# Optimization experiments

Measured on AMD Instinct MI355X. Metric: run time of the kernel, lower is better.

Reference implementation:

```python
import jax, jax.numpy as jnp
import numpy as np

WS = 7  # window size


def _rel_pos_index(ws):
    coords = np.stack(np.meshgrid(np.arange(ws), np.arange(ws), indexing='ij')).reshape(2, -1)
    rel = (coords[:, :, None] - coords[:, None, :]).transpose(1, 2, 0)  # (N,N,2)
    rel[..., 0] += ws - 1
    rel[..., 1] += ws - 1
    rel[..., 0] *= 2 * ws - 1
    return jnp.asarray(rel.sum(-1))  # (N,N) int


def setup_inputs() -> dict:
    key = jax.random.key(0)
    ks = jax.random.split(key, 10)
    B, DIM, H, W, NH = 16, 256, 56, 56, 8
    HD = DIM // NH
    x = jax.random.normal(ks[0], (B, DIM, H, W), jnp.float32)
    qkv_w = jax.random.normal(ks[1], (DIM, 3 * DIM), jnp.float32) * 0.02
    qkv_b = jnp.zeros((3 * DIM,), jnp.float32)
    fc_w = jax.random.normal(ks[2], (9, 3 * NH), jnp.float32) * 0.1
    fc_b = jnp.zeros((9,), jnp.float32)
    base = np.zeros((9, 3, 3), np.float32)
    for i in range(9):
        base[i, i // 3, i % 3] = 1.0
    dep_w = jnp.asarray(np.broadcast_to(base, (DIM, 9, 3, 3)).copy()) \
        + jax.random.normal(ks[3], (DIM, 9, 3, 3), jnp.float32) * 0.01
    proj_w = jax.random.normal(ks[4], (DIM, DIM), jnp.float32) * 0.02
    proj_b = jnp.zeros((DIM,), jnp.float32)
    rpb_table = jax.random.normal(ks[5], ((2 * WS - 1) * (2 * WS - 1), NH), jnp.float32) * 0.02
    rate1 = jnp.full((1,), 0.5, jnp.float32)
    rate2 = jnp.full((1,), 0.5, jnp.float32)
    return dict(x=x, qkv_w=qkv_w, qkv_b=qkv_b, fc_w=fc_w, fc_b=fc_b, dep_w=dep_w,
                proj_w=proj_w, proj_b=proj_b, rpb_table=rpb_table, rate1=rate1, rate2=rate2)


def reference(x, qkv_w, qkv_b, fc_w, fc_b, dep_w, proj_w, proj_b, rpb_table, rate1, rate2):
    B, DIM, H, W = x.shape
    NH = fc_w.shape[1] // 3
    HD = DIM // NH
    N = WS * WS
    xp = jnp.transpose(x, (0, 2, 3, 1))              # (B,H,W,C)
    qkv = xp @ qkv_w + qkv_b                          # (B,H,W,3C)

    # ----- conv branch -----
    f_all = qkv.reshape(B, H * W, 3 * NH, HD)         # (B,HW,3NH,HD)
    fc_out = jnp.einsum('oc,bncd->bnod', fc_w, f_all) + fc_b[None, None, :, None]  # (B,HW,9,HD)
    # torch channel layout: (B, HD, 9, HW) -> (B, 9*HD, H, W) with hd-major ordering
    f_conv = jnp.transpose(fc_out, (0, 3, 2, 1)).reshape(B, 9 * HD, H, W)
    out_conv = jax.lax.conv_general_dilated(
        f_conv, dep_w, window_strides=(1, 1), padding=((1, 1), (1, 1)),
        feature_group_count=HD, dimension_numbers=('NCHW', 'OIHW', 'NCHW'))  # (B,C,H,W)
    out_conv = jnp.transpose(out_conv, (0, 2, 3, 1))  # (B,H,W,C)

    # ----- window attention branch -----
    w = qkv.reshape(B, H // WS, WS, W // WS, WS, 3 * DIM)
    w = jnp.transpose(w, (0, 1, 3, 2, 4, 5)).reshape(-1, N, 3 * DIM)  # (B_,N,3C)
    B_ = w.shape[0]
    w = w.reshape(B_, N, 3, NH, HD)
    q, k, v = jnp.transpose(w, (2, 0, 3, 1, 4))       # each (B_,NH,N,HD)
    scale = HD ** -0.5
    attn = jnp.einsum('bhnd,bhmd->bhnm', q * scale, k)  # (B_,NH,N,N)
    idx = _rel_pos_index(WS)
    bias = jnp.transpose(rpb_table[idx.reshape(-1)].reshape(N, N, NH), (2, 0, 1))  # (NH,N,N)
    attn = jax.nn.softmax(attn + bias[None], axis=-1)
    o = jnp.einsum('bhnm,bhmd->bnhd', attn, v).reshape(B_, N, DIM)
    o = o @ proj_w.T + proj_b                          # torch Linear: y = x W^T + b
    o = o.reshape(B_, WS, WS, DIM)
    o = o.reshape(B, H // WS, W // WS, WS, WS, DIM)
    o = jnp.transpose(o, (0, 1, 3, 2, 4, 5)).reshape(B, H, W, DIM)

    out = rate1 * o + rate2 * out_conv
    return jnp.transpose(out, (0, 3, 1, 2))           # (B,C,H,W)
```

## Files before the change

### kernel.cpp

```cpp
#include <hip/hip_runtime.h>

#define BATCH 16
#define DIM 256
#define HH 56
#define WW 56
#define HWP 3136
#define M_TOT 50176
#define NQKV 768
#define NHEADS 8
#define HDIM 32
#define NWIN 49
#define QKV_BYTES   77070336ull
#define XT_OFF      77070336ull
#define XT_BYTES    25690112ull
#define WQT_OFF    102760448ull
#define PWB_OFF    103153664ull
#define FCONV_OFF  103284736ull
#define BIAS_OFF   132186112ull

typedef float f32x4 __attribute__((ext_vector_type(4)));
typedef short short8 __attribute__((ext_vector_type(8)));
typedef unsigned short ushort4v __attribute__((ext_vector_type(4)));

__device__ __forceinline__ short f2bf(float f) {
    unsigned u = __float_as_uint(f);
    u += 0x7fffu + ((u >> 16) & 1u);
    return (short)(u >> 16);
}
__device__ __forceinline__ float bf2f(unsigned short u) {
    return __uint_as_float(((unsigned)u) << 16);
}
__device__ __forceinline__ unsigned pack2bf(float lo, float hi) {
    unsigned ul = __float_as_uint(lo); ul += 0x7fffu + ((ul >> 16) & 1u);
    unsigned uh = __float_as_uint(hi); uh += 0x7fffu + ((uh >> 16) & 1u);
    return (ul >> 16) | (uh & 0xffff0000u);
}
__device__ __forceinline__ int div7(int n) { return (n * 9363) >> 16; }

__device__ __forceinline__ void gld16(const unsigned short* g, unsigned short* l) {
    __builtin_amdgcn_global_load_lds(
        (const __attribute__((address_space(1))) void*)g,
        (__attribute__((address_space(3))) void*)l, 16, 0, 0);
}

__global__ __launch_bounds__(256) void xpose_kernel(const float* __restrict__ x,
                                                    unsigned short* __restrict__ xt) {
    __shared__ unsigned short tls[64 * 448];
    const int tid = threadIdx.x;
    const int p0 = blockIdx.x * 448;
    const int k0 = blockIdx.y * 64;
    const int b  = blockIdx.z;
    const float* xb = x + ((size_t)b * DIM + k0) * HWP + p0;
    #pragma unroll
    for (int pass = 0; pass < 28; ++pass) {
        int idx = tid + pass * 256;
        int ch = idx / 112, px4 = idx - ch * 112;
        float4 v = *(const float4*)(xb + (size_t)ch * HWP + px4 * 4);
        int px4s = px4 ^ ((ch >> 3) & 7);
        ushort4v s;
        s[0] = (unsigned short)f2bf(v.x); s[1] = (unsigned short)f2bf(v.y);
        s[2] = (unsigned short)f2bf(v.z); s[3] = (unsigned short)f2bf(v.w);
        *(ushort4v*)&tls[ch * 448 + px4s * 4] = s;
    }
    __syncthreads();
    unsigned short* xto = xt + ((size_t)b * HWP + p0) * DIM + k0;
    #pragma unroll
    for (int q = 0; q < 14; ++q) {
        int idx = tid + q * 256;
        int px = idx >> 3, j8 = (idx & 7) * 8;
        int key = (j8 >> 3) & 7;
        int pxs = ((px >> 2) ^ key) * 4 + (px & 3);
        unsigned r[4];
        #pragma unroll
        for (int jj = 0; jj < 4; ++jj) {
            unsigned lo = tls[(j8 + 2 * jj) * 448 + pxs];
            unsigned hi = tls[(j8 + 2 * jj + 1) * 448 + pxs];
            r[jj] = lo | (hi << 16);
        }
        uint4 o; o.x = r[0]; o.y = r[1]; o.z = r[2]; o.w = r[3];
        *(uint4*)(xto + (size_t)px * DIM + j8) = o;
    }
}

__global__ __launch_bounds__(256) void prep_kernel(const float* __restrict__ wq,
                                                   const float* __restrict__ pw,
                                                   const float* __restrict__ rpb,
                                                   unsigned short* __restrict__ wqt,
                                                   unsigned short* __restrict__ pwb,
                                                   float* __restrict__ biasT) {
    const int tid = threadIdx.x;
    const int bid = blockIdx.x;
    if (bid < 48) {
        __shared__ float t[64][65];
        const int j0 = (bid >> 2) * 64, k0 = (bid & 3) * 64;
        #pragma unroll
        for (int kk = tid >> 6; kk < 64; kk += 4)
            t[kk][tid & 63] = wq[(size_t)(k0 + kk) * NQKV + j0 + (tid & 63)];
        __syncthreads();
        const int jj = tid >> 2, c16 = (tid & 3) * 16;
        unsigned short* dst = wqt + (size_t)(j0 + jj) * DIM + k0 + c16;
        #pragma unroll
        for (int i = 0; i < 16; ++i) dst[i] = (unsigned short)f2bf(t[c16 + i][jj]);
    } else if (bid < 64) {
        const int base = (bid - 48) * 4096 + tid;
        #pragma unroll
        for (int i = 0; i < 16; ++i)
            pwb[base + i * 256] = (unsigned short)f2bf(pw[base + i * 256]);
    } else {
        const int h = bid - 64;
        #pragma unroll
        for (int i = 0; i < 16; ++i) {
            int idx = tid + i * 256;
            int n = idx >> 6, m = idx & 63;
            float v = -1e30f;
            if (n < 49 && m < 49) {
                int nd = div7(n), md = div7(m);
                int ii = (nd - md + 6) * 13 + ((n - nd * 7) - (m - md * 7) + 6);
                v = rpb[ii * NHEADS + h] * 1.4426950408889634f;
            }
            biasT[h * 4096 + idx] = v;
        }
    }
}

__global__ __launch_bounds__(256) void qkv_gemm(const unsigned short* __restrict__ xt,
                                                const unsigned short* __restrict__ wqt,
                                                const float* __restrict__ bq,
                                                unsigned short* __restrict__ qkv) {
    __shared__ __attribute__((aligned(16))) short A_lds[2][128 * 32];
    __shared__ __attribute__((aligned(16))) short B_lds[2][128 * 32];
    const int bidx = blockIdx.x;
    const int wg = (bidx & 7) * 294 + (bidx >> 3);
    const int jt = wg % 6, mt = wg / 6;
    const int m0 = mt * 128, j0 = jt * 128;

    const int tid = threadIdx.x;
    const int lane = tid & 63;
    const int wave = tid >> 6;
    const int wr = wave >> 1, wc = wave & 1;
    const int r = lane & 15, q = lane >> 4;

    const unsigned short* aG[2];
    const unsigned short* bG[2];
    int lbase[2];
    #pragma unroll
    for (int t = 0; t < 2; ++t) {
        int ci = wave * 128 + t * 64 + lane;
        int srow = ci >> 2;
        int kgrp = (ci & 3) ^ (srow & 3);
        aG[t] = xt  + (size_t)(m0 + srow) * DIM + kgrp * 8;
        bG[t] = wqt + (size_t)(j0 + srow) * DIM + kgrp * 8;
        lbase[t] = (wave * 128 + t * 64) * 8;
    }

    f32x4 acc[4][4];
    #pragma unroll
    for (int i = 0; i < 4; ++i)
        #pragma unroll
        for (int j = 0; j < 4; ++j) acc[i][j] = (f32x4){0.f, 0.f, 0.f, 0.f};

    #pragma unroll
    for (int t = 0; t < 2; ++t) {
        gld16(aG[t], (unsigned short*)&A_lds[0][lbase[t]]);
        gld16(bG[t], (unsigned short*)&B_lds[0][lbase[t]]);
    }
    __syncthreads();

    #pragma unroll
    for (int k = 0; k < 8; ++k) {
        const int buf = k & 1;
        if (k < 7) {
            const int k0 = (k + 1) * 32;
            #pragma unroll
            for (int t = 0; t < 2; ++t) {
                gld16(aG[t] + k0, (unsigned short*)&A_lds[buf ^ 1][lbase[t]]);
                gld16(bG[t] + k0, (unsigned short*)&B_lds[buf ^ 1][lbase[t]]);
            }
        }
        short8 af[4], bfr[4];
        #pragma unroll
        for (int f = 0; f < 4; ++f) {
            int mrow = wr * 64 + f * 16 + r;
            af[f] = *(const short8*)&A_lds[buf][mrow * 32 + 8 * (q ^ (mrow & 3))];
            int nrow = wc * 64 + f * 16 + r;
            bfr[f] = *(const short8*)&B_lds[buf][nrow * 32 + 8 * (q ^ (nrow & 3))];
        }
        #pragma unroll
        for (int fm = 0; fm < 4; ++fm)
            #pragma unroll
            for (int fj = 0; fj < 4; ++fj)
                acc[fm][fj] = __builtin_amdgcn_mfma_f32_16x16x32_bf16(
                    af[fm], bfr[fj], acc[fm][fj], 0, 0, 0);
        __syncthreads();
    }

    #pragma unroll
    for (int fm = 0; fm < 4; ++fm) {
        const int mbase = m0 + wr * 64 + fm * 16 + q * 4;
        #pragma unroll
        for (int fj = 0; fj < 4; ++fj) {
            const int j = j0 + wc * 64 + fj * 16 + r;
            const float bias = bq[j];
            unsigned short* op = qkv + (size_t)mbase * NQKV + j;
            #pragma unroll
            for (int rg = 0; rg < 4; ++rg)
                op[(size_t)rg * NQKV] = (unsigned short)f2bf(acc[fm][fj][rg] + bias);
        }
    }
}

__global__ __launch_bounds__(256) void fc_kernel(const unsigned short* __restrict__ qkv,
                                                 const float* __restrict__ fc_w,
                                                 const float* __restrict__ fc_b,
                                                 unsigned short* __restrict__ fconv) {
    __shared__ unsigned short f[16 * 768];
    __shared__ float ob[16][289];
    __shared__ float w[9][24];
    __shared__ float bsh[9];
    const int tid = threadIdx.x;
    if (tid < 216) w[tid / 24][tid % 24] = fc_w[tid];
    if (tid < 9) bsh[tid] = fc_b[tid];
    const int p0 = blockIdx.x * 16;
    const int b  = blockIdx.y;
    const uint4* src = (const uint4*)(qkv + ((size_t)b * HWP + p0) * NQKV);
    uint4* dstf = (uint4*)f;
    #pragma unroll
    for (int i = 0; i < 6; ++i) dstf[tid + i * 256] = src[tid + i * 256];
    __syncthreads();
    #pragma unroll
    for (int it = 0; it < 2; ++it) {
        const int item = tid + it * 256;
        const int pp = item >> 5, g = item & 31;
        const unsigned short* fr = f + pp * 768 + g;
        float acc[9];
        #pragma unroll
        for (int o = 0; o < 9; ++o) acc[o] = bsh[o];
        #pragma unroll
        for (int c = 0; c < 24; ++c) {
            float v = bf2f(fr[c * 32]);
            #pragma unroll
            for (int o = 0; o < 9; ++o) acc[o] += w[o][c] * v;
        }
        #pragma unroll
        for (int o = 0; o < 9; ++o) ob[pp][g * 9 + o] = acc[o];
    }
    __syncthreads();
    unsigned short* og = fconv + (size_t)b * 288 * HWP + p0;
    for (int i = tid; i < 288 * 16; i += 256) {
        int ch = i >> 4, pp = i & 15;
        og[(size_t)ch * HWP + pp] = (unsigned short)f2bf(ob[pp][ch]);
    }
}

__global__ __launch_bounds__(256) void conv_kernel(const unsigned short* __restrict__ fconv,
                                                   const float* __restrict__ dep_w,
                                                   const float* __restrict__ rate2p,
                                                   float* __restrict__ out) {
    __shared__ unsigned short hal[9][10][64];
    __shared__ float wfl[81][8];
    const int tid = threadIdx.x;
    const int strip = blockIdx.x;
    const int g = blockIdx.y, b = blockIdx.z;

    for (int i = tid; i < 648; i += 256) {
        int ok = i >> 3, c8 = i & 7;
        wfl[ok][c8] = dep_w[(size_t)(g * 8 + c8) * 81 + ok];
    }
    const unsigned short* fp = fconv + ((size_t)b * 288 + g * 9) * HWP;
    const int y0 = strip * 8 - 1;
    for (int i = tid; i < 5760; i += 256) {
        int col = i & 63;
        int rest = i >> 6;
        int o = rest / 10, y = rest - o * 10;
        int gy = y0 + y, gx = col - 1;
        unsigned short v = 0;
        if (gy >= 0 && gy < HH && (unsigned)gx < WW)
            v = fp[(size_t)o * HWP + gy * WW + gx];
        hal[o][y][col] = v;
    }
    __syncthreads();

    const int x = tid & 63;
    const int w = tid >> 6;
    const int e = x & ~1;
    const bool odd = (x & 1) != 0;
    float acc[2][8] = {};
    for (int o = 0; o < 9; ++o) {
        float V[4][3];
        #pragma unroll
        for (int h = 0; h < 4; ++h) {
            const unsigned short* hr = &hal[o][2 * w + h][e];
            unsigned D0 = *(const unsigned*)hr;
            unsigned D1 = *(const unsigned*)(hr + 2);
            float a0 = __uint_as_float(D0 << 16);
            float a1 = __uint_as_float(D0 & 0xffff0000u);
            float a2 = __uint_as_float(D1 << 16);
            float a3 = __uint_as_float(D1 & 0xffff0000u);
            V[h][0] = odd ? a1 : a0;
            V[h][1] = odd ? a2 : a1;
            V[h][2] = odd ? a3 : a2;
        }
        #pragma unroll
        for (int ky = 0; ky < 3; ++ky)
            #pragma unroll
            for (int kx = 0; kx < 3; ++kx) {
                f32x4 w0 = *(const f32x4*)&wfl[o * 9 + ky * 3 + kx][0];
                f32x4 w1 = *(const f32x4*)&wfl[o * 9 + ky * 3 + kx][4];
                #pragma unroll
                for (int j = 0; j < 2; ++j) {
                    const float vv = V[j + ky][kx];
                    acc[j][0] += vv * w0[0]; acc[j][1] += vv * w0[1];
                    acc[j][2] += vv * w0[2]; acc[j][3] += vv * w0[3];
                    acc[j][4] += vv * w1[0]; acc[j][5] += vv * w1[1];
                    acc[j][6] += vv * w1[2]; acc[j][7] += vv * w1[3];
                }
            }
    }
    if (x < WW) {
        const float r2 = rate2p[0];
        #pragma unroll
        for (int j = 0; j < 2; ++j) {
            const int y = strip * 8 + 2 * w + j;
            #pragma unroll
            for (int c8 = 0; c8 < 8; ++c8)
                out[((size_t)b * DIM + g * 8 + c8) * HWP + y * WW + x] = r2 * acc[j][c8];
        }
    }
}

__global__ __launch_bounds__(512) void attn_kernel(const unsigned short* __restrict__ qkv,
                                                   const float* __restrict__ biasT,
                                                   unsigned short* __restrict__ obuf) {
    __shared__ __attribute__((aligned(16))) short PL[8 * 16 * 72];
    const int tid = threadIdx.x;
    const int win = blockIdx.x;
    const int b = win >> 6, wrw = win & 63;
    const int wy = wrw >> 3, wx = wrw & 7;
    const size_t wbase = (size_t)b * HWP + (size_t)(wy * 7) * WW + wx * 7;

    const int lane = tid & 63;
    const int h = tid >> 6;
    const int c = lane & 15, qg = lane >> 4;

    short8 aq[4], bk[4];
    #pragma unroll
    for (int f = 0; f < 4; ++f) {
        int t = f * 16 + c; if (t > 48) t = 48;
        const int tq = div7(t), tr = t - tq * 7;
        const unsigned short* base = qkv + (wbase + tq * WW + tr) * NQKV + h * 32 + qg * 8;
        aq[f] = *(const short8*)base;
        bk[f] = *(const short8*)(base + 256);
    }
    short8 bv[2][2];
    #pragma unroll
    for (int ks = 0; ks < 2; ++ks)
        #pragma unroll
        for (int i = 0; i < 8; ++i) {
            int pix = ks * 32 + qg * 8 + i; if (pix > 48) pix = 48;
            const int pd = div7(pix);
            const unsigned short* vp = qkv + (wbase + pd * WW + (pix - pd * 7)) * NQKV
                                           + 512 + h * 32 + c;
            bv[ks][0][i] = (short)vp[0];
            bv[ks][1][i] = (short)vp[16];
        }

    const float cst = 0.25503766727f;
    const float* bt = biasT + h * 4096;
    short* pw = PL + h * 16 * 72;

    #pragma unroll
    for (int fm = 0; fm < 4; ++fm) {
        f32x4 s[4];
        #pragma unroll
        for (int fj = 0; fj < 4; ++fj)
            s[fj] = __builtin_amdgcn_mfma_f32_16x16x32_bf16(aq[fm], bk[fj],
                                                            (f32x4){0.f,0.f,0.f,0.f}, 0, 0, 0);
        float p[4][4];
        #pragma unroll
        for (int reg = 0; reg < 4; ++reg) {
            const float* brow = bt + (fm * 16 + qg * 4 + reg) * 64;
            #pragma unroll
            for (int fj = 0; fj < 4; ++fj)
                p[fj][reg] = exp2f(s[fj][reg] * cst + brow[fj * 16 + c]);
        }
        float inv[4];
        #pragma unroll
        for (int reg = 0; reg < 4; ++reg) {
            float sum = (p[0][reg] + p[1][reg]) + (p[2][reg] + p[3][reg]);
            sum += __shfl_xor(sum, 1);
            sum += __shfl_xor(sum, 2);
            sum += __shfl_xor(sum, 4);
            sum += __shfl_xor(sum, 8);
            inv[reg] = 1.0f / sum;
        }
        #pragma unroll
        for (int fj = 0; fj < 4; ++fj)
            #pragma unroll
            for (int reg = 0; reg < 4; ++reg) {
                float v = p[fj][reg];
                float o = __shfl_xor(v, 1);
                unsigned packed = (c & 1) ? pack2bf(o, v) : pack2bf(v, o);
                if ((c & 1) == 0)
                    *(unsigned*)&pw[(qg * 4 + reg) * 72 + fj * 16 + c] = packed;
            }
        short8 ap0 = *(const short8*)&pw[c * 72 + 0 * 32 + qg * 8];
        short8 ap1 = *(const short8*)&pw[c * 72 + 1 * 32 + qg * 8];
        #pragma unroll
        for (int fo = 0; fo < 2; ++fo) {
            f32x4 o4 = __builtin_amdgcn_mfma_f32_16x16x32_bf16(ap0, bv[0][fo],
                                                               (f32x4){0.f,0.f,0.f,0.f}, 0, 0, 0);
            o4 = __builtin_amdgcn_mfma_f32_16x16x32_bf16(ap1, bv[1][fo], o4, 0, 0, 0);
            #pragma unroll
            for (int reg = 0; reg < 4; ++reg) {
                int n = fm * 16 + qg * 4 + reg;
                if (n < 49) {
                    int nd = div7(n), nm = n - nd * 7;
                    obuf[(wbase + nd * WW + nm) * DIM + h * 32 + fo * 16 + c] =
                        (unsigned short)f2bf(o4[reg] * inv[reg]);
                }
            }
        }
    }
}

__global__ __launch_bounds__(256) void proj_gemm(const unsigned short* __restrict__ obuf,
                                                 const unsigned short* __restrict__ pwb,
                                                 const float* __restrict__ pb,
                                                 const float* __restrict__ rate1p,
                                                 float* __restrict__ out) {
    __shared__ __attribute__((aligned(16))) short M_lds[2][128 * 32];
    __shared__ __attribute__((aligned(16))) short C_lds[2][128 * 32];
    const int bidx = blockIdx.x;
    const int wg = (bidx & 7) * 98 + (bidx >> 3);
    const int ct = wg & 1, mt = wg >> 1;
    const int m0 = mt * 128, c0 = ct * 128;

    const int tid = threadIdx.x;
    const int lane = tid & 63;
    const int wave = tid >> 6;
    const int wr = wave >> 1, wc = wave & 1;
    const int r = lane & 15, q = lane >> 4;

    const unsigned short* mG[2];
    const unsigned short* cG[2];
    int lbase[2];
    #pragma unroll
    for (int t = 0; t < 2; ++t) {
        int ci = wave * 128 + t * 64 + lane;
        int srow = ci >> 2;
        int kgrp = (ci & 3) ^ (srow & 3);
        mG[t] = obuf + (size_t)(m0 + srow) * DIM + kgrp * 8;
        cG[t] = pwb  + (size_t)(c0 + srow) * DIM + kgrp * 8;
        lbase[t] = (wave * 128 + t * 64) * 8;
    }

    f32x4 acc[4][4];
    #pragma unroll
    for (int i = 0; i < 4; ++i)
        #pragma unroll
        for (int j = 0; j < 4; ++j) acc[i][j] = (f32x4){0.f, 0.f, 0.f, 0.f};

    #pragma unroll
    for (int t = 0; t < 2; ++t) {
        gld16(mG[t], (unsigned short*)&M_lds[0][lbase[t]]);
        gld16(cG[t], (unsigned short*)&C_lds[0][lbase[t]]);
    }
    __syncthreads();

    #pragma unroll
    for (int k = 0; k < 8; ++k) {
        const int buf = k & 1;
        if (k < 7) {
            const int k0 = (k + 1) * 32;
            #pragma unroll
            for (int t = 0; t < 2; ++t) {
                gld16(mG[t] + k0, (unsigned short*)&M_lds[buf ^ 1][lbase[t]]);
                gld16(cG[t] + k0, (unsigned short*)&C_lds[buf ^ 1][lbase[t]]);
            }
        }
        short8 cf[4], mf[4];
        #pragma unroll
        for (int f = 0; f < 4; ++f) {
            int crow = wr * 64 + f * 16 + r;
            cf[f] = *(const short8*)&C_lds[buf][crow * 32 + 8 * (q ^ (crow & 3))];
            int mrow = wc * 64 + f * 16 + r;
            mf[f] = *(const short8*)&M_lds[buf][mrow * 32 + 8 * (q ^ (mrow & 3))];
        }
        #pragma unroll
        for (int fc = 0; fc < 4; ++fc)
            #pragma unroll
            for (int fm2 = 0; fm2 < 4; ++fm2)
                acc[fc][fm2] = __builtin_amdgcn_mfma_f32_16x16x32_bf16(
                    cf[fc], mf[fm2], acc[fc][fm2], 0, 0, 0);
        __syncthreads();
    }

    const float r1 = rate1p[0];
    size_t boff[4];
    #pragma unroll
    for (int fm2 = 0; fm2 < 4; ++fm2) {
        int mb = m0 + wc * 64 + fm2 * 16 + r;
        boff[fm2] = (size_t)(mb / HWP) * DIM * HWP + (mb % HWP);
    }
    #pragma unroll
    for (int fc = 0; fc < 4; ++fc) {
        #pragma unroll
        for (int reg = 0; reg < 4; ++reg) {
            const int cc = c0 + wr * 64 + fc * 16 + q * 4 + reg;
            const float bias = pb[cc];
            #pragma unroll
            for (int fm2 = 0; fm2 < 4; ++fm2) {
                float* dst = out + boff[fm2] + (size_t)cc * HWP;
                *dst = *dst + r1 * (acc[fc][fm2][reg] + bias);
            }
        }
    }
}

extern "C" void kernel_launch(void* const* d_in, const int* in_sizes, int n_in,
                              void* d_out, int out_size, void* d_ws, size_t ws_size,
                              hipStream_t stream) {
    const float* x      = (const float*)d_in[0];
    const float* qkv_w  = (const float*)d_in[1];
    const float* qkv_b  = (const float*)d_in[2];
    const float* fc_w   = (const float*)d_in[3];
    const float* fc_b   = (const float*)d_in[4];
    const float* dep_w  = (const float*)d_in[5];
    const float* proj_w = (const float*)d_in[6];
    const float* proj_b = (const float*)d_in[7];
    const float* rpb    = (const float*)d_in[8];
    const float* rate1  = (const float*)d_in[9];
    const float* rate2  = (const float*)d_in[10];
    float* out = (float*)d_out;

    unsigned short* qkv   = (unsigned short*)d_ws;
    unsigned short* xt    = (unsigned short*)((char*)d_ws + XT_OFF);
    unsigned short* wqt   = (unsigned short*)((char*)d_ws + WQT_OFF);
    unsigned short* pwb   = (unsigned short*)((char*)d_ws + PWB_OFF);
    unsigned short* fconv = (unsigned short*)((char*)d_ws + FCONV_OFF);
    float*          biasT = (float*)((char*)d_ws + BIAS_OFF);
    unsigned short* obuf  = fconv;

    xpose_kernel<<<dim3(7, 4, BATCH), 256, 0, stream>>>(x, xt);
    prep_kernel<<<dim3(72), 256, 0, stream>>>(qkv_w, proj_w, rpb, wqt, pwb, biasT);
    qkv_gemm<<<dim3(2352), 256, 0, stream>>>(xt, wqt, qkv_b, qkv);
    fc_kernel<<<dim3(HWP / 16, BATCH), 256, 0, stream>>>(qkv, fc_w, fc_b, fconv);
    conv_kernel<<<dim3(7, 32, BATCH), 256, 0, stream>>>(fconv, dep_w, rate2, out);
    attn_kernel<<<dim3(1024), 512, 0, stream>>>(qkv, biasT, obuf);
    proj_gemm<<<dim3(784), 256, 0, stream>>>(obuf, pwb, proj_b, rate1, out);
}
```

Baseline: 230.5 us.

## Switch conv branch to fp16 with packed dot2 over input channels

The intermediate conv features are now stored as fp16 instead of bf16. The halo tile is re-laid out in shared memory as channel-innermost (pixel-major) so pairs of input channels can be fed to v_dot2 f16 instructions. Weights are pre-packed into fp16 pairs by an extra prep block and read from global memory instead of shared memory. This halves the FMA instruction count and removes the bf16 unpacking, at the cost of fp16 range and precision and more register pressure from holding 60 packed values per thread.

```diff
diff --git a/kernel.cpp b/kernel.cpp
--- a/kernel.cpp
+++ b/kernel.cpp
@@ -17,10 +17,13 @@
 #define PWB_OFF    103153664ull
 #define FCONV_OFF  103284736ull
 #define BIAS_OFF   132186112ull
+#define WDOT_OFF   132317184ull
 
 typedef float f32x4 __attribute__((ext_vector_type(4)));
+typedef float f32x2 __attribute__((ext_vector_type(2)));
 typedef short short8 __attribute__((ext_vector_type(8)));
 typedef unsigned short ushort4v __attribute__((ext_vector_type(4)));
+typedef _Float16 h16x2 __attribute__((ext_vector_type(2)));
 
 __device__ __forceinline__ short f2bf(float f) {
     unsigned u = __float_as_uint(f);
@@ -34,6 +37,12 @@
     unsigned ul = __float_as_uint(lo); ul += 0x7fffu + ((ul >> 16) & 1u);
     unsigned uh = __float_as_uint(hi); uh += 0x7fffu + ((uh >> 16) & 1u);
     return (ul >> 16) | (uh & 0xffff0000u);
+}
+__device__ __forceinline__ unsigned short f2h(float f) {
+    union { _Float16 h; unsigned short u; } cv; cv.h = (_Float16)f; return cv.u;
+}
+__device__ __forceinline__ h16x2 as_h2(unsigned u) {
+    union { unsigned u; h16x2 h; } cv; cv.u = u; return cv.h;
 }
 __device__ __forceinline__ int div7(int n) { return (n * 9363) >> 16; }
 
@@ -85,9 +94,11 @@
 __global__ __launch_bounds__(256) void prep_kernel(const float* __restrict__ wq,
                                                    const float* __restrict__ pw,
                                                    const float* __restrict__ rpb,
+                                                   const float* __restrict__ dep_w,
                                                    unsigned short* __restrict__ wqt,
                                                    unsigned short* __restrict__ pwb,
-                                                   float* __restrict__ biasT) {
+                                                   float* __restrict__ biasT,
+                                                   unsigned* __restrict__ wdot) {
     const int tid = threadIdx.x;
     const int bid = blockIdx.x;
     if (bid < 48) {
@@ -106,7 +117,7 @@
         #pragma unroll
         for (int i = 0; i < 16; ++i)
             pwb[base + i * 256] = (unsigned short)f2bf(pw[base + i * 256]);
-    } else {
+    } else if (bid < 72) {
         const int h = bid - 64;
         #pragma unroll
         for (int i = 0; i < 16; ++i) {
@@ -120,6 +131,16 @@
             }
             biasT[h * 4096 + idx] = v;
         }
+    } else {
+        for (int i = tid; i < 11520; i += 256) {
+            int g = i / 360, rem = i - g * 360;
+            int c8 = rem / 45, rem2 = rem - c8 * 45;
+            int kykx = rem2 / 5, p = rem2 - kykx * 5;
+            int ch = g * 8 + c8;
+            float w0 = dep_w[(size_t)ch * 81 + (2 * p) * 9 + kykx];
+            float w1 = (p < 4) ? dep_w[(size_t)ch * 81 + (2 * p + 1) * 9 + kykx] : 0.f;
+            wdot[i] = (unsigned)f2h(w0) | ((unsigned)f2h(w1) << 16);
+        }
     }
 }
 
@@ -248,74 +269,64 @@
     unsigned short* og = fconv + (size_t)b * 288 * HWP + p0;
     for (int i = tid; i < 288 * 16; i += 256) {
         int ch = i >> 4, pp = i & 15;
-        og[(size_t)ch * HWP + pp] = (unsigned short)f2bf(ob[pp][ch]);
+        og[(size_t)ch * HWP + pp] = f2h(ob[pp][ch]);
     }
 }
 
 __global__ __launch_bounds__(256) void conv_kernel(const unsigned short* __restrict__ fconv,
-                                                   const float* __restrict__ dep_w,
+                                                   const unsigned* __restrict__ wdot,
                                                    const float* __restrict__ rate2p,
                                                    float* __restrict__ out) {
-    __shared__ unsigned short hal[9][10][64];
-    __shared__ float wfl[81][8];
+    __shared__ unsigned short hal[10 * 66 * 10];
     const int tid = threadIdx.x;
     const int strip = blockIdx.x;
     const int g = blockIdx.y, b = blockIdx.z;
 
-    for (int i = tid; i < 648; i += 256) {
-        int ok = i >> 3, c8 = i & 7;
-        wfl[ok][c8] = dep_w[(size_t)(g * 8 + c8) * 81 + ok];
-    }
     const unsigned short* fp = fconv + ((size_t)b * 288 + g * 9) * HWP;
     const int y0 = strip * 8 - 1;
-    for (int i = tid; i < 5760; i += 256) {
-        int col = i & 63;
-        int rest = i >> 6;
-        int o = rest / 10, y = rest - o * 10;
-        int gy = y0 + y, gx = col - 1;
+    for (int i = tid; i < 5800; i += 256) {
+        int o = i / 580, rem = i - o * 580;
+        int y = rem / 58, xx = rem - y * 58;
+        int gy = y0 + y, gx = xx - 1;
         unsigned short v = 0;
-        if (gy >= 0 && gy < HH && (unsigned)gx < WW)
+        if (o < 9 && gy >= 0 && gy < HH && (unsigned)gx < WW)
             v = fp[(size_t)o * HWP + gy * WW + gx];
-        hal[o][y][col] = v;
+        hal[(y * 66 + xx) * 10 + o] = v;
     }
     __syncthreads();
 
     const int x = tid & 63;
     const int w = tid >> 6;
-    const int e = x & ~1;
-    const bool odd = (x & 1) != 0;
+    const int xc = x < 55 ? x : 55;
+
+    unsigned D[4][3][5];
+    #pragma unroll
+    for (int h = 0; h < 4; ++h)
+        #pragma unroll
+        for (int kx = 0; kx < 3; ++kx) {
+            const int base = ((2 * w + h) * 66 + xc + kx) * 10;
+            #pragma unroll
+            for (int p = 0; p < 5; ++p)
+                D[h][kx][p] = *(const unsigned*)&hal[base + 2 * p];
+        }
+
+    const unsigned* wg = wdot + g * 360;
     float acc[2][8] = {};
-    for (int o = 0; o < 9; ++o) {
-        float V[4][3];
-        #pragma unroll
-        for (int h = 0; h < 4; ++h) {
-            const unsigned short* hr = &hal[o][2 * w + h][e];
-            unsigned D0 = *(const unsigned*)hr;
-            unsigned D1 = *(const unsigned*)(hr + 2);
-            float a0 = __uint_as_float(D0 << 16);
-            float a1 = __uint_as_float(D0 & 0xffff0000u);
-            float a2 = __uint_as_float(D1 << 16);
-            float a3 = __uint_as_float(D1 & 0xffff0000u);
-            V[h][0] = odd ? a1 : a0;
-            V[h][1] = odd ? a2 : a1;
-            V[h][2] = odd ? a3 : a2;
-        }
+    #pragma unroll
+    for (int c8 = 0; c8 < 8; ++c8)
         #pragma unroll
         for (int ky = 0; ky < 3; ++ky)
             #pragma unroll
-            for (int kx = 0; kx < 3; ++kx) {
-                f32x4 w0 = *(const f32x4*)&wfl[o * 9 + ky * 3 + kx][0];
-                f32x4 w1 = *(const f32x4*)&wfl[o * 9 + ky * 3 + kx][4];
+            for (int kx = 0; kx < 3; ++kx)
                 #pragma unroll
-                for (int j = 0; j < 2; ++j) {
-                    const float vv = V[j + ky][kx];
-                    acc[j][0] += vv * w0[0]; acc[j][1] += vv * w0[1];
-                    acc[j][2] += vv * w0[2]; acc[j][3] += vv * w0[3];
-                    acc[j][4] += vv * w1[0]; acc[j][5] += vv * w1[1];
-                    acc[j][6] += vv * w1[2]; acc[j][7] += vv * w1[3];
+                for (int p = 0; p < 5; ++p) {
+                    h16x2 wh = as_h2(wg[c8 * 45 + (ky * 3 + kx) * 5 + p]);
+                    acc[0][c8] = __builtin_amdgcn_fdot2(as_h2(D[ky][kx][p]), wh,
+                                                        acc[0][c8], false);
+                    acc[1][c8] = __builtin_amdgcn_fdot2(as_h2(D[ky + 1][kx][p]), wh,
+                                                        acc[1][c8], false);
                 }
-            }
-    }
+
     if (x < WW) {
         const float r2 = rate2p[0];
         #pragma unroll
@@ -539,13 +550,14 @@
     unsigned short* pwb   = (unsigned short*)((char*)d_ws + PWB_OFF);
     unsigned short* fconv = (unsigned short*)((char*)d_ws + FCONV_OFF);
     float*          biasT = (float*)((char*)d_ws + BIAS_OFF);
+    unsigned*       wdot  = (unsigned*)((char*)d_ws + WDOT_OFF);
     unsigned short* obuf  = fconv;
 
     xpose_kernel<<<dim3(7, 4, BATCH), 256, 0, stream>>>(x, xt);
-    prep_kernel<<<dim3(72), 256, 0, stream>>>(qkv_w, proj_w, rpb, wqt, pwb, biasT);
+    prep_kernel<<<dim3(73), 256, 0, stream>>>(qkv_w, proj_w, rpb, dep_w, wqt, pwb, biasT, wdot);
     qkv_gemm<<<dim3(2352), 256, 0, stream>>>(xt, wqt, qkv_b, qkv);
     fc_kernel<<<dim3(HWP / 16, BATCH), 256, 0, stream>>>(qkv, fc_w, fc_b, fconv);
-    conv_kernel<<<dim3(7, 32, BATCH), 256, 0, stream>>>(fconv, dep_w, rate2, out);
+    conv_kernel<<<dim3(7, 32, BATCH), 256, 0, stream>>>(fconv, wdot, rate2, out);
     attn_kernel<<<dim3(1024), 512, 0, stream>>>(qkv, biasT, obuf);
     proj_gemm<<<dim3(784), 256, 0, stream>>>(obuf, pwb, proj_b, rate1, out);
 }
```

Measured after the change: 242.4 us. 5.2% more time.
